# Kernel optimization log

Hardware: AMD Instinct MI355X
Metric: run time of the kernel (lower is better)

## Reference

```python
import jax, jax.numpy as jnp
import numpy as np

N_CLASS, N_SUPPORT, N_QUERY = 64, 5, 64
D_IN, C, WIN = 1024, 128, 5
D = C * WIN * WIN  # 3200, fine-encoder output dim


def setup_inputs() -> dict:
    key = jax.random.key(0)
    ks = jax.random.split(key, 6)
    s = 0.02  # weight init scale
    return {
        "xs": jax.random.normal(ks[0], (N_CLASS, N_SUPPORT, D_IN), jnp.float32),
        "xq": jax.random.normal(ks[1], (N_CLASS, N_QUERY, D_IN), jnp.float32),
        "W_share": jax.random.normal(ks[2], (D_IN, D), jnp.float32) * s,
        "b_share": jnp.zeros((D,), jnp.float32),
        "W_att": jax.random.normal(ks[3], (C, C), jnp.float32) * s,
        "b_att": jnp.zeros((C,), jnp.float32),
        "W_fine": jax.random.normal(ks[4], (D, D), jnp.float32) * s,
        "b_fine": jnp.zeros((D,), jnp.float32),
    }


def reference(xs, xq, W_share, b_share, W_att, b_att, W_fine, b_fine):
    n_class, n_support = xs.shape[0], xs.shape[1]
    n_query = xq.shape[1]
    ns = n_class * n_support

    # concat support + query, run shared encoder
    x = jnp.concatenate([xs.reshape(ns, -1), xq.reshape(n_class * n_query, -1)], axis=0)
    z_share = jax.nn.relu(x @ W_share + b_share)            # [N, D]
    z4 = z_share.reshape(-1, C, WIN, WIN)

    # attention head: spatial mean -> linear -> per-channel logits
    z_att = z4.mean(axis=(2, 3)) @ W_att + b_att            # [N, C]

    diag_c = jax.nn.softmax(z_att[:ns].mean(axis=0)) * C    # [C]
    w = jnp.repeat(diag_c, WIN * WIN)                       # [D] diagonal of learned metric

    # fine encoder (flatten + linear)
    z = z_share @ W_fine + b_fine                           # [N, D]
    z_proto = z[:ns].reshape(n_class, n_support, -1).mean(axis=1)  # [n_class, D]
    zq = z[ns:]                                             # [n, D]

    # attentionMetric with diagonal metric == weighted squared distance:
    # dists[i,j] = sum_d w_d (zq_i - proto_j)^2, expanded to avoid the n*m*d diff tensor
    q2 = (zq * zq) @ w                                      # [n]
    p2 = (z_proto * z_proto) @ w                            # [m]
    cross = (zq * w) @ z_proto.T                            # [n, m]
    dists = q2[:, None] + p2[None, :] - 2.0 * cross         # [n, m]

    log_p_y = jax.nn.log_softmax(-dists, axis=1).reshape(n_class, n_query, n_class)
    target = jnp.arange(n_class)
    tgt = jnp.broadcast_to(target[:, None, None], (n_class, n_query, 1))
    loss_val = -jnp.take_along_axis(log_p_y, tgt, axis=2).mean()
    y_hat = jnp.argmax(log_p_y, axis=2)
    acc_val = (y_hat == target[:, None]).astype(jnp.float32).mean()
    return loss_val, acc_val
```

## Files before the change

### kernel.cpp

```cpp
#include <hip/hip_runtime.h>
#include <math.h>

#define N_CLASS 64
#define N_SUPPORT 5
#define N_QUERY 64
#define D_IN 1024
#define C_CH 128
#define WIN 5
#define D_FEAT 3200
#define NS 320
#define NQ 4096
#define M_ROWS 4416
#define M_PAD 4480

#define ZP_SLICE  (N_CLASS * D_FEAT)
#define GT_SLICE  (128 * D_FEAT)
#define CR_SLICE  (NQ * 128)
#define NKS       10
#define LOSS_BLKS (NQ / 4)

#define PREP_X   4480
#define PREP_WS  800
#define CONV64   2500
#define GEMM8_BLKS (35 * 25)

#define WS_SCALE    64.0f
#define WS_INVSCALE 0.015625f

#define WS_XF8      0u
#define WS_WSF8     4718592u
#define WS_ZSB      8126464u
#define WS_WFB      36388864u
#define WS_WFTB     56868864u
#define WS_ARENA    77348864u
#define WS_UB       98320384u
#define WS_YB       99139584u
#define WS_GT       99958784u
#define WS_WV       100777984u
#define WS_P2       100790784u
#define WS_CVEC     100791296u
#define WS_LPART    100791808u
#define WS_UPOOL    100800128u


typedef __bf16 bf16x8 __attribute__((ext_vector_type(8)));
typedef __bf16 bf16x4 __attribute__((ext_vector_type(4)));
typedef float floatx4 __attribute__((ext_vector_type(4)));
typedef __attribute__((address_space(1))) const void* gptr_t;
typedef __attribute__((address_space(3))) void* lptr_t;

__device__ __forceinline__ float waveReduceSum(float v) {
    for (int off = 32; off > 0; off >>= 1) v += __shfl_xor(v, off, 64);
    return v;
}

__global__ __launch_bounds__(256) void prep_kernel(const float* __restrict__ xs,
                                                   const float* __restrict__ xq,
                                                   const float* __restrict__ W_share,
                                                   unsigned char* __restrict__ Xf8,
                                                   unsigned char* __restrict__ Wsf8)
{
    __shared__ float tile[64][65];
    const int b = blockIdx.x;
    const int t = threadIdx.x;

    if (b < PREP_X) {
        const int e = (b * 256 + t) * 4;
        const int row = e >> 10;
        const int col = e & 1023;
        float4 v = make_float4(0.f, 0.f, 0.f, 0.f);
        if (row < NS)          v = *(const float4*)(xs + (size_t)row * D_IN + col);
        else if (row < M_ROWS) v = *(const float4*)(xq + (size_t)(row - NS) * D_IN + col);
        int p = __builtin_amdgcn_cvt_pk_fp8_f32(v.x, v.y, 0, false);
        p     = __builtin_amdgcn_cvt_pk_fp8_f32(v.z, v.w, p, true);
        const int ocol = col ^ (((row >> 1) & 1) << 3);
        *(int*)(Xf8 + (size_t)row * D_IN + ocol) = p;
        return;
    }
    const int tx = t & 63;
    const int ty = t >> 6;
    const int tb = b - PREP_X;
    const int n0 = (tb % 50) * 64;
    const int k0 = (tb / 50) * 64;
#pragma unroll
    for (int i = ty; i < 64; i += 4)
        tile[i][tx] = W_share[(size_t)(k0 + i) * D_FEAT + n0 + tx];
    __syncthreads();
#pragma unroll
    for (int i = ty; i < 64; i += 4) {
        const int p = __builtin_amdgcn_cvt_pk_fp8_f32(tile[tx][i] * WS_SCALE, 0.f,
                                                      0, false);
        const int n = n0 + i;
        const int k = (k0 + tx) ^ (((n >> 1) & 1) << 3);
        Wsf8[(size_t)n * D_IN + k] = (unsigned char)(p & 0xff);
    }
}

__global__ __launch_bounds__(256, 3) void gemm_fp8_128(const unsigned char* __restrict__ A,
                                                       const unsigned char* __restrict__ Bt,
                                                       const float* __restrict__ bias,
                                                       __bf16* __restrict__ out_bf)
{
    __shared__ __align__(16) unsigned char smem[49152];

    const int t    = threadIdx.x;
    const int lane = t & 63;
    const int w    = t >> 6;
    const int wm   = w >> 1;
    const int wn   = w & 1;

    const int bx = blockIdx.x % 25;
    const int by = blockIdx.x / 25;
    const int bm = by * 128;
    const int bn = bx * 128;

    const int q    = lane >> 4;
    const int r16  = lane & 15;
    const int m3   = (r16 >> 1) & 7;
    const int off0 = (q ^ m3) * 8;

    const int rowA = (wm * 64 + r16) * 64;
    const int rowB = (wn * 64 + r16) * 64;

    const int srow  = t >> 2;
    const int sunit = 16 * ((t & 3) ^ ((srow >> 2) & 3));

    const unsigned char* gA = A  + (size_t)(bm + srow) * D_IN + sunit;
    const unsigned char* gB = Bt + (size_t)(bn + srow) * D_IN + sunit;

    auto stage = [&](int uu, int slot) {
        const unsigned char* ga = gA + uu * 64;
        const unsigned char* gb = gB + uu * 64;
        unsigned char* l = smem + slot * 16384 + t * 16;
        __builtin_amdgcn_global_load_lds((gptr_t)ga,           (lptr_t)l,            16, 0, 0);
        __builtin_amdgcn_global_load_lds((gptr_t)(ga + 65536), (lptr_t)(l + 4096),   16, 0, 0);
        __builtin_amdgcn_global_load_lds((gptr_t)gb,           (lptr_t)(l + 8192),   16, 0, 0);
        __builtin_amdgcn_global_load_lds((gptr_t)(gb + 65536), (lptr_t)(l + 12288),  16, 0, 0);
    };

    floatx4 acc[4][4] = {};
    long av0[4], bv0[4], av1[4], bv1[4];

    auto ld16 = [&](const unsigned char* sa) {
#pragma unroll
        for (int mi = 0; mi < 4; ++mi)
            av0[mi] = *(const long*)(sa + rowA + mi * 1024 + off0);
#pragma unroll
        for (int ni = 0; ni < 4; ++ni)
            bv0[ni] = *(const long*)(sa + 8192 + rowB + ni * 1024 + off0);
#pragma unroll
        for (int mi = 0; mi < 4; ++mi)
            av1[mi] = *(const long*)(sa + rowA + mi * 1024 + (off0 ^ 32));
#pragma unroll
        for (int ni = 0; ni < 4; ++ni)
            bv1[ni] = *(const long*)(sa + 8192 + rowB + ni * 1024 + (off0 ^ 32));
    };
    auto mfma32 = [&]() {
        __builtin_amdgcn_s_setprio(1);
#pragma unroll
        for (int mi = 0; mi < 4; ++mi)
#pragma unroll
            for (int ni = 0; ni < 4; ++ni)
                acc[mi][ni] = __builtin_amdgcn_mfma_f32_16x16x32_fp8_fp8(
                    av0[mi], bv0[ni], acc[mi][ni], 0, 0, 0);
#pragma unroll
        for (int mi = 0; mi < 4; ++mi)
#pragma unroll
            for (int ni = 0; ni < 4; ++ni)
                acc[mi][ni] = __builtin_amdgcn_mfma_f32_16x16x32_fp8_fp8(
                    av1[mi], bv1[ni], acc[mi][ni], 0, 0, 0);
        __builtin_amdgcn_s_setprio(0);
    };

    stage(0, 0);
    stage(1, 1);

    for (int u = 0; u < 14; ++u) {
        const unsigned char* sa = smem + (u % 3) * 16384;
        asm volatile("s_waitcnt vmcnt(4)" ::: "memory");
        __builtin_amdgcn_s_barrier();
        ld16(sa);
        stage(u + 2, (u + 2) % 3);
        asm volatile("s_waitcnt lgkmcnt(0)" ::: "memory");
        mfma32();
    }
    {
        const unsigned char* sa = smem + (14 % 3) * 16384;
        asm volatile("s_waitcnt vmcnt(4)" ::: "memory");
        __builtin_amdgcn_s_barrier();
        ld16(sa);
        asm volatile("s_waitcnt lgkmcnt(0)" ::: "memory");
        mfma32();
    }
    {
        const unsigned char* sa = smem + (15 % 3) * 16384;
        asm volatile("s_waitcnt vmcnt(0)" ::: "memory");
        __builtin_amdgcn_s_barrier();
        ld16(sa);
        asm volatile("s_waitcnt lgkmcnt(0)" ::: "memory");
        mfma32();
    }

    __syncthreads();
    float bcol[4];
#pragma unroll
    for (int ni = 0; ni < 4; ++ni) bcol[ni] = bias[bn + wn * 64 + ni * 16 + r16];
    const int ebase = (wm * 64 + q * 4) * 256 + wn * 128 + r16 * 2;
#pragma unroll
    for (int mi = 0; mi < 4; ++mi)
#pragma unroll
        for (int ni = 0; ni < 4; ++ni) {
            const int cb2 = (ni ^ q) << 5;
#pragma unroll
            for (int reg = 0; reg < 4; ++reg) {
                float v = acc[mi][ni][reg] * WS_INVSCALE + bcol[ni];
                v = fmaxf(v, 0.f);
                *(__bf16*)(smem + ebase + mi * 4096 + reg * 256 + cb2) = (__bf16)v;
            }
        }
    __syncthreads();
#pragma unroll
    for (int ps = 0; ps < 8; ++ps) {
        const int idx  = ps * 256 + t;
        const int row  = idx >> 4;
        const int grow = bm + row;
        if (grow < M_ROWS) {
            const int lb = row * 256 + (((idx & 15) << 4) ^ (((row >> 2) & 3) << 5));
            const int4 d = *(const int4*)(smem + lb);
            *(int4*)((char*)out_bf + ((size_t)grow * D_FEAT + bn + (idx & 15) * 8) * 2) = d;
        }
    }
}

__global__ __launch_bounds__(256) void gemm_bf16(const __bf16* __restrict__ A,
                                                 const __bf16* __restrict__ Bt,
                                                 const float* __restrict__ bias,
                                                 __bf16* __restrict__ out_bf,
                                                 float* __restrict__ out_f32,
                                                 int N, int strideK, int kIters,
                                                 int Mout, int relu, int sliceStride,
                                                 int nbx, int nby, int colLimit,
                                                 const float* __restrict__ attUpool,
                                                 const float* __restrict__ W_att,
                                                 const float* __restrict__ b_att,
                                                 float* __restrict__ wvec)
{
    __shared__ __align__(16) char smem[65536];
    const int t = threadIdx.x;

    if (attUpool != nullptr && blockIdx.x == gridDim.x - 1) {
        float* sW   = (float*)smem;
        float* s_pm = (float*)(smem + 16384);
        float* s_at = (float*)(smem + 16384 + 512);
        float* s_dg = (float*)(smem + 16384 + 1024);
        if (t < C_CH) {
            float a = 0.f;
            for (int p = 0; p < N_CLASS; ++p) a += attUpool[(size_t)p * C_CH + t];
            s_pm[t] = a * (1.0f / (N_CLASS * 25));
        }
        __syncthreads();
        float acc = (t < C_CH) ? b_att[t] : 0.f;
#pragma unroll
        for (int qtr = 0; qtr < 4; ++qtr) {
            const float4* src = (const float4*)(W_att + qtr * 32 * C_CH);
            float4* dst = (float4*)sW;
#pragma unroll
            for (int i = 0; i < 4; ++i) dst[i * 256 + t] = src[i * 256 + t];
            __syncthreads();
            if (t < C_CH) {
#pragma unroll
                for (int k = 0; k < 32; ++k)
                    acc += s_pm[qtr * 32 + k] * sW[k * C_CH + t];
            }
            __syncthreads();
        }
        if (t < C_CH) s_at[t] = acc;
        __syncthreads();
        if (t < C_CH) {
            float m = -INFINITY;
            for (int k = 0; k < C_CH; ++k) m = fmaxf(m, s_at[k]);
            float s = 0.f;
            for (int k = 0; k < C_CH; ++k) s += expf(s_at[k] - m);
            s_dg[t] = expf(acc - m) / s * (float)C_CH;
        }
        __syncthreads();
        for (int j = t; j < D_FEAT; j += 256) wvec[j] = s_dg[j / 25];
        return;
    }

    int bx, by, ks;
    {
        const int nbxy = nbx * nby;
        ks = blockIdx.x / nbxy;
        const int b = blockIdx.x - ks * nbxy;
        const int fg = nbx >> 3;
        const int full = fg * 8 * nby;
        if (b < full) {
            const int g = b / (8 * nby);
            const int r = b - g * 8 * nby;
            bx = g * 8 + (r & 7);
            by = r >> 3;
        } else {
            const int rem = nbx - fg * 8;
            const int r = b - full;
            bx = fg * 8 + r % rem;
            by = r / rem;
        }
    }

    const int lane = t & 63;
    const int w    = t >> 6;
    const int wm   = w >> 1;
    const int wn   = w & 1;
    const int bm   = by * 128;
    const int bn   = bx * 128;

    const int q    = lane >> 4;
    const int r16  = lane & 15;
    const int sw   = (r16 >> 1) & 3;
    const int cA   = (q ^ sw) * 8;

    const int srow   = w * 16 + (lane >> 2);
    const int sglob8 = (((lane & 3) ^ ((lane >> 3) & 3))) * 8;

    const int kBase = ks * kIters * 64;
    floatx4 acc[4][4] = {};

    auto stageb = [&](int ki, char* base) {
        const int k0 = kBase + ki * 64;
#pragma unroll
        for (int s = 0; s < 2; ++s) {
#pragma unroll
            for (int j = 0; j < 2; ++j) {
                const __bf16* ga = A  + (size_t)(bm + j * 64 + srow) * strideK
                                      + k0 + s * 32 + sglob8;
                const __bf16* gb = Bt + (size_t)(bn + j * 64 + srow) * strideK
                                      + k0 + s * 32 + sglob8;
                char* la = base +         s * 8192 + (j * 256 + w * 64) * 16;
                char* lb = base + 16384 + s * 8192 + (j * 256 + w * 64) * 16;
                __builtin_amdgcn_global_load_lds((gptr_t)ga, (lptr_t)la, 16, 0, 0);
                __builtin_amdgcn_global_load_lds((gptr_t)gb, (lptr_t)lb, 16, 0, 0);
            }
        }
    };

    stageb(0, smem);
    for (int ki = 0; ki < kIters; ++ki) {
        char* base = smem + (ki & 1) * 32768;
        __syncthreads();
        if (ki + 1 < kIters) stageb(ki + 1, smem + ((ki + 1) & 1) * 32768);

#pragma unroll
        for (int s = 0; s < 2; ++s) {
            const __bf16* sAe = (const __bf16*)(base +         s * 8192);
            const __bf16* sBe = (const __bf16*)(base + 16384 + s * 8192);
            bf16x8 av[4], bv[4];
#pragma unroll
            for (int mi = 0; mi < 4; ++mi)
                av[mi] = *(const bf16x8*)(sAe + ((wm * 64 + mi * 16 + r16) * 32 + cA));
#pragma unroll
            for (int ni = 0; ni < 4; ++ni)
                bv[ni] = *(const bf16x8*)(sBe + ((wn * 64 + ni * 16 + r16) * 32 + cA));
#pragma unroll
            for (int mi = 0; mi < 4; ++mi)
#pragma unroll
                for (int ni = 0; ni < 4; ++ni)
                    acc[mi][ni] = __builtin_amdgcn_mfma_f32_16x16x32_bf16(
                        av[mi], bv[ni], acc[mi][ni], 0, 0, 0);
        }
    }

#pragma unroll
    for (int ni = 0; ni < 4; ++ni) {
        const int col = bn + wn * 64 + ni * 16 + r16;
        if (col < colLimit) {
            const float bcol = sliceStride ? 0.f : bias[col];
#pragma unroll
            for (int mi = 0; mi < 4; ++mi) {
#pragma unroll
                for (int reg = 0; reg < 4; ++reg) {
                    const int row = bm + wm * 64 + mi * 16 + q * 4 + reg;
                    if (row < Mout) {
                        if (sliceStride) {
                            out_f32[(size_t)ks * sliceStride + (size_t)row * N + col] =
                                acc[mi][ni][reg];
                        } else {
                            float v = acc[mi][ni][reg] + bcol;
                            if (relu) v = fmaxf(v, 0.f);
                            if (out_f32) out_f32[(size_t)row * N + col] = v;
                            else         out_bf [(size_t)row * N + col] = (__bf16)v;
                        }
                    }
                }
            }
        }
    }
}

__global__ __launch_bounds__(256) void ut_conv_kernel(const __bf16* __restrict__ z_share,
                                                      const float* __restrict__ W_fine,
                                                      __bf16* __restrict__ u,
                                                      float* __restrict__ upool,
                                                      __bf16* __restrict__ Wfb,
                                                      __bf16* __restrict__ WfTb)
{
    __shared__ __align__(16) char smem_u[16640];
    const int b = blockIdx.x;
    const int t = threadIdx.x;

    if (b >= 128) {
        float (*tile)[65] = (float(*)[65])smem_u;
        const int tb = b - 128;
        const int tx = t & 63;
        const int ty = t >> 6;
        const int n0 = (tb % 50) * 64;
        const int k0 = (tb / 50) * 64;
#pragma unroll
        for (int i = ty; i < 64; i += 4) {
            const float v = W_fine[(size_t)(k0 + i) * D_FEAT + n0 + tx];
            Wfb[(size_t)(k0 + i) * D_FEAT + n0 + tx] = (__bf16)v;
            tile[i][tx] = v;
        }
        __syncthreads();
#pragma unroll
        for (int i = ty; i < 64; i += 4)
            WfTb[(size_t)(n0 + i) * D_FEAT + k0 + tx] = (__bf16)tile[tx][i];
        return;
    }

    float* srow_ = (float*)smem_u;
    const int p = b;
    if (p >= N_CLASS) {
        for (int k = t; k < D_FEAT; k += 256) u[(size_t)p * D_FEAT + k] = (__bf16)0.f;
        return;
    }
    const __bf16* base = z_share + (size_t)(p * N_SUPPORT) * D_FEAT;
    for (int k = t; k < D_FEAT; k += 256) {
        float s = 0.f;
#pragma unroll
        for (int ss = 0; ss < N_SUPPORT; ++ss) s += (float)base[(size_t)ss * D_FEAT + k];
        s *= (1.0f / N_SUPPORT);
        u[(size_t)p * D_FEAT + k] = (__bf16)s;
        srow_[k] = s;
    }
    __syncthreads();
    if (t < C_CH) {
        float pool = 0.f;
#pragma unroll
        for (int win = 0; win < 25; ++win) pool += srow_[t * 25 + win];
        upool[(size_t)p * C_CH + t] = pool;
    }
}

__global__ __launch_bounds__(256) void y_kernel(const float* __restrict__ zp_part,
                                                const float* __restrict__ wv,
                                                const float* __restrict__ bf,
                                                __bf16* __restrict__ y,
                                                float* __restrict__ p2,
                                                float* __restrict__ cvec)
{
    __shared__ float s_red2[8];
    const int p = blockIdx.x;
    const int t = threadIdx.x;
    if (p >= N_CLASS) {
        for (int j = t; j < D_FEAT; j += 256) y[(size_t)p * D_FEAT + j] = (__bf16)0.f;
        return;
    }
    float s2 = 0.f, sc = 0.f;
    for (int j = t; j < D_FEAT; j += 256) {
        float zpf = bf[j];
#pragma unroll
        for (int ss = 0; ss < NKS; ++ss)
            zpf += zp_part[(size_t)ss * ZP_SLICE + (size_t)p * D_FEAT + j];
        const float wj = wv[j];
        y[(size_t)p * D_FEAT + j] = (__bf16)(wj * zpf);
        s2 += wj * zpf * zpf;
        sc += bf[j] * wj * zpf;
    }
    s2 = waveReduceSum(s2);
    sc = waveReduceSum(sc);
    const int lane = t & 63, wid = t >> 6;
    if (lane == 0) { s_red2[wid] = s2; s_red2[4 + wid] = sc; }
    __syncthreads();
    if (t == 0) {
        p2[p]   = s_red2[0] + s_red2[1] + s_red2[2] + s_red2[3];
        cvec[p] = s_red2[4] + s_red2[5] + s_red2[6] + s_red2[7];
    }
}

__global__ __launch_bounds__(256) void gtsum_kernel(const float* __restrict__ gp,
                                                    __bf16* __restrict__ Gt)
{
    const int i4 = blockIdx.x * 256 + threadIdx.x;
    if (i4 >= GT_SLICE / 4) return;
    float4 s = make_float4(0.f, 0.f, 0.f, 0.f);
#pragma unroll
    for (int ss = 0; ss < NKS; ++ss) {
        const float4 v = *(const float4*)(gp + (size_t)ss * GT_SLICE + i4 * 4);
        s.x += v.x; s.y += v.y; s.z += v.z; s.w += v.w;
    }
    bf16x4 o = { (__bf16)s.x, (__bf16)s.y, (__bf16)s.z, (__bf16)s.w };
    *(bf16x4*)(Gt + (size_t)i4 * 4) = o;
}

__global__ __launch_bounds__(256) void loss_kernel(const float* __restrict__ cross_part,
                                                   const float* __restrict__ p2,
                                                   const float* __restrict__ cvec,
                                                   float* __restrict__ lpart)
{
    __shared__ float s_l[4], s_a[4];
    const int t = threadIdx.x;
    const int lane = t & 63, wid = t >> 6;
    const int i = blockIdx.x * 4 + wid;
    float cr = 0.f;
#pragma unroll
    for (int ss = 0; ss < NKS; ++ss)
        cr += cross_part[(size_t)ss * CR_SLICE + (size_t)i * 128 + lane];
    const float neg = 2.0f * (cr + cvec[lane]) - p2[lane];
    float m = neg;
    for (int off = 32; off > 0; off >>= 1) m = fmaxf(m, __shfl_xor(m, off, 64));
    float e = expf(neg - m);
    float ssum = e;
    for (int off = 32; off > 0; off >>= 1) ssum += __shfl_xor(ssum, off, 64);
    const float lse = m + logf(ssum);
    const int tcls = i >> 6;
    const float negt = __shfl(neg, tcls, 64);
    float v = -neg; int bi = lane;
    for (int off = 32; off > 0; off >>= 1) {
        const float ov = __shfl_xor(v, off, 64);
        const int   oi = __shfl_xor(bi, off, 64);
        if (ov < v || (ov == v && oi < bi)) { v = ov; bi = oi; }
    }
    if (lane == 0) { s_l[wid] = lse - negt; s_a[wid] = (bi == tcls) ? 1.0f : 0.0f; }
    __syncthreads();
    if (t == 0) {
        lpart[blockIdx.x]             = s_l[0] + s_l[1] + s_l[2] + s_l[3];
        lpart[LOSS_BLKS + blockIdx.x] = s_a[0] + s_a[1] + s_a[2] + s_a[3];
    }
}

__global__ __launch_bounds__(256) void writeout_kernel(const float* __restrict__ lpart,
                                                       float* __restrict__ out)
{
    __shared__ float s_red2[8];
    const int t = threadIdx.x;
    float l = 0.f, a = 0.f;
    for (int k = t; k < LOSS_BLKS; k += 256) {
        l += lpart[k];
        a += lpart[LOSS_BLKS + k];
    }
    l = waveReduceSum(l);
    a = waveReduceSum(a);
    const int lane = t & 63, wid = t >> 6;
    if (lane == 0) { s_red2[wid] = l; s_red2[4 + wid] = a; }
    __syncthreads();
    if (t == 0) {
        out[0] = (s_red2[0] + s_red2[1] + s_red2[2] + s_red2[3]) * (1.0f / NQ);
        out[1] = (s_red2[4] + s_red2[5] + s_red2[6] + s_red2[7]) * (1.0f / NQ);
    }
}

extern "C" void kernel_launch(void* const* d_in, const int* in_sizes, int n_in,
                              void* d_out, int out_size, void* d_ws, size_t ws_size,
                              hipStream_t stream)
{
    const float* xs      = (const float*)d_in[0];
    const float* xq      = (const float*)d_in[1];
    const float* W_share = (const float*)d_in[2];
    const float* b_share = (const float*)d_in[3];
    const float* W_att   = (const float*)d_in[4];
    const float* b_att   = (const float*)d_in[5];
    const float* W_fine  = (const float*)d_in[6];
    const float* b_fine  = (const float*)d_in[7];
    float* out = (float*)d_out;

    char* ws = (char*)d_ws;
    unsigned char* Xf8  = (unsigned char*)(ws + WS_XF8);
    unsigned char* Wsf8 = (unsigned char*)(ws + WS_WSF8);
    __bf16* Zsb     = (__bf16*)(ws + WS_ZSB);
    __bf16* Wfb     = (__bf16*)(ws + WS_WFB);
    __bf16* WfTb    = (__bf16*)(ws + WS_WFTB);
    float*  arena   = (float*) (ws + WS_ARENA);
    float*  zp_part = arena;
    float*  gt_part = arena;
    float*  cr_part = arena;
    __bf16* ub      = (__bf16*)(ws + WS_UB);
    __bf16* yb      = (__bf16*)(ws + WS_YB);
    __bf16* Gt      = (__bf16*)(ws + WS_GT);
    float*  wv      = (float*) (ws + WS_WV);
    float*  p2v     = (float*) (ws + WS_P2);
    float*  cvec    = (float*) (ws + WS_CVEC);
    float*  lpart   = (float*) (ws + WS_LPART);
    float*  upool   = (float*) (ws + WS_UPOOL);

    prep_kernel<<<PREP_X + PREP_WS, 256, 0, stream>>>(xs, xq, W_share, Xf8, Wsf8);

    gemm_fp8_128<<<GEMM8_BLKS, 256, 0, stream>>>(Xf8, Wsf8, b_share, Zsb);

    ut_conv_kernel<<<128 + CONV64, 256, 0, stream>>>(Zsb, W_fine, ub, upool,
                                                     Wfb, WfTb);

    gemm_bf16<<<25 * NKS + 1, 256, 0, stream>>>(
        ub, WfTb, nullptr, nullptr, zp_part,
        D_FEAT, D_FEAT, 5, N_CLASS, 0, ZP_SLICE, 25, 1, D_FEAT,
        upool, W_att, b_att, wv);

    y_kernel<<<128, 256, 0, stream>>>(zp_part, wv, b_fine, yb, p2v, cvec);

    gemm_bf16<<<25 * NKS, 256, 0, stream>>>(
        yb, Wfb, nullptr, nullptr, gt_part,
        D_FEAT, D_FEAT, 5, 128, 0, GT_SLICE, 25, 1, D_FEAT,
        nullptr, nullptr, nullptr, nullptr);

    gtsum_kernel<<<(GT_SLICE / 4 + 255) / 256, 256, 0, stream>>>(gt_part, Gt);

    gemm_bf16<<<32 * NKS, 256, 0, stream>>>(
        Zsb + (size_t)NS * D_FEAT, Gt, nullptr, nullptr, cr_part,
        128, D_FEAT, 5, NQ, 0, CR_SLICE, 1, 32, 64,
        nullptr, nullptr, nullptr, nullptr);

    loss_kernel<<<LOSS_BLKS, 256, 0, stream>>>(cr_part, p2v, cvec, lpart);

    writeout_kernel<<<1, 256, 0, stream>>>(lpart, out);
}
```

Baseline: 220.0 us.

## Switch bf16 GEMM to triple-buffered 32-wide K stages with explicit waitcnt

Restructures the bf16 GEMM main loop from double-buffered 64-wide K steps into a three-slot ring of 32-wide K steps, prefetching two stages ahead. Explicit vmcnt/lgkmcnt waits and a raw barrier replace __syncthreads, so loads for stage u+2 are issued while stage u is computed. Shared memory drops from 64KB to 48KB, which may allow more resident blocks. The trade-off is twice as many barriers per K range and reliance on hand-written waitcnt counts being correct.

```diff
diff --git a/kernel.cpp b/kernel.cpp
--- a/kernel.cpp
+++ b/kernel.cpp
@@ -245,7 +245,7 @@
                                                  const float* __restrict__ b_att,
                                                  float* __restrict__ wvec)
 {
-    __shared__ __align__(16) char smem[65536];
+    __shared__ __align__(16) char smem[49152];
     const int t = threadIdx.x;
 
     if (attUpool != nullptr && blockIdx.x == gridDim.x - 1) {
@@ -323,51 +323,59 @@
     const int srow   = w * 16 + (lane >> 2);
     const int sglob8 = (((lane & 3) ^ ((lane >> 3) & 3))) * 8;
 
-    const int kBase = ks * kIters * 64;
+    const int kBase = ks * kIters * 32;
     floatx4 acc[4][4] = {};
 
-    auto stageb = [&](int ki, char* base) {
-        const int k0 = kBase + ki * 64;
-#pragma unroll
-        for (int s = 0; s < 2; ++s) {
-#pragma unroll
-            for (int j = 0; j < 2; ++j) {
-                const __bf16* ga = A  + (size_t)(bm + j * 64 + srow) * strideK
-                                      + k0 + s * 32 + sglob8;
-                const __bf16* gb = Bt + (size_t)(bn + j * 64 + srow) * strideK
-                                      + k0 + s * 32 + sglob8;
-                char* la = base +         s * 8192 + (j * 256 + w * 64) * 16;
-                char* lb = base + 16384 + s * 8192 + (j * 256 + w * 64) * 16;
-                __builtin_amdgcn_global_load_lds((gptr_t)ga, (lptr_t)la, 16, 0, 0);
-                __builtin_amdgcn_global_load_lds((gptr_t)gb, (lptr_t)lb, 16, 0, 0);
-            }
+    auto stageb = [&](int ki, int slot) {
+        const int k0 = kBase + ki * 32;
+        char* base = smem + slot * 16384;
+#pragma unroll
+        for (int j = 0; j < 2; ++j) {
+            const __bf16* ga = A  + (size_t)(bm + j * 64 + srow) * strideK
+                                  + k0 + sglob8;
+            const __bf16* gb = Bt + (size_t)(bn + j * 64 + srow) * strideK
+                                  + k0 + sglob8;
+            char* la = base +        j * 4096 + w * 1024;
+            char* lb = base + 8192 + j * 4096 + w * 1024;
+            __builtin_amdgcn_global_load_lds((gptr_t)ga, (lptr_t)la, 16, 0, 0);
+            __builtin_amdgcn_global_load_lds((gptr_t)gb, (lptr_t)lb, 16, 0, 0);
         }
     };
 
-    stageb(0, smem);
-    for (int ki = 0; ki < kIters; ++ki) {
-        char* base = smem + (ki & 1) * 32768;
-        __syncthreads();
-        if (ki + 1 < kIters) stageb(ki + 1, smem + ((ki + 1) & 1) * 32768);
-
-#pragma unroll
-        for (int s = 0; s < 2; ++s) {
-            const __bf16* sAe = (const __bf16*)(base +         s * 8192);
-            const __bf16* sBe = (const __bf16*)(base + 16384 + s * 8192);
-            bf16x8 av[4], bv[4];
-#pragma unroll
-            for (int mi = 0; mi < 4; ++mi)
-                av[mi] = *(const bf16x8*)(sAe + ((wm * 64 + mi * 16 + r16) * 32 + cA));
+    bf16x8 av[4], bv[4];
+    auto ldfrags = [&](const char* base) {
+        const __bf16* sAe = (const __bf16*)base;
+        const __bf16* sBe = (const __bf16*)(base + 8192);
+#pragma unroll
+        for (int mi = 0; mi < 4; ++mi)
+            av[mi] = *(const bf16x8*)(sAe + ((wm * 64 + mi * 16 + r16) * 32 + cA));
+#pragma unroll
+        for (int ni = 0; ni < 4; ++ni)
+            bv[ni] = *(const bf16x8*)(sBe + ((wn * 64 + ni * 16 + r16) * 32 + cA));
+    };
+    auto mfma16 = [&]() {
+#pragma unroll
+        for (int mi = 0; mi < 4; ++mi)
 #pragma unroll
             for (int ni = 0; ni < 4; ++ni)
-                bv[ni] = *(const bf16x8*)(sBe + ((wn * 64 + ni * 16 + r16) * 32 + cA));
-#pragma unroll
-            for (int mi = 0; mi < 4; ++mi)
-#pragma unroll
-                for (int ni = 0; ni < 4; ++ni)
-                    acc[mi][ni] = __builtin_amdgcn_mfma_f32_16x16x32_bf16(
-                        av[mi], bv[ni], acc[mi][ni], 0, 0, 0);
-        }
+                acc[mi][ni] = __builtin_amdgcn_mfma_f32_16x16x32_bf16(
+                    av[mi], bv[ni], acc[mi][ni], 0, 0, 0);
+    };
+
+    stageb(0, 0);
+    stageb(1, 1);
+
+    for (int u = 0; u < kIters; ++u) {
+        const char* base = smem + (u % 3) * 16384;
+        if (u + 1 < kIters)
+            asm volatile("s_waitcnt vmcnt(4)" ::: "memory");
+        else
+            asm volatile("s_waitcnt vmcnt(0)" ::: "memory");
+        __builtin_amdgcn_s_barrier();
+        ldfrags(base);
+        if (u + 2 < kIters) stageb(u + 2, (u + 2) % 3);
+        asm volatile("s_waitcnt lgkmcnt(0)" ::: "memory");
+        mfma16();
     }
 
 #pragma unroll
@@ -602,21 +610,21 @@
 
     gemm_bf16<<<25 * NKS + 1, 256, 0, stream>>>(
         ub, WfTb, nullptr, nullptr, zp_part,
-        D_FEAT, D_FEAT, 5, N_CLASS, 0, ZP_SLICE, 25, 1, D_FEAT,
+        D_FEAT, D_FEAT, 10, N_CLASS, 0, ZP_SLICE, 25, 1, D_FEAT,
         upool, W_att, b_att, wv);
 
     y_kernel<<<128, 256, 0, stream>>>(zp_part, wv, b_fine, yb, p2v, cvec);
 
     gemm_bf16<<<25 * NKS, 256, 0, stream>>>(
         yb, Wfb, nullptr, nullptr, gt_part,
-        D_FEAT, D_FEAT, 5, 128, 0, GT_SLICE, 25, 1, D_FEAT,
+        D_FEAT, D_FEAT, 10, 128, 0, GT_SLICE, 25, 1, D_FEAT,
         nullptr, nullptr, nullptr, nullptr);
 
     gtsum_kernel<<<(GT_SLICE / 4 + 255) / 256, 256, 0, stream>>>(gt_part, Gt);
 
     gemm_bf16<<<32 * NKS, 256, 0, stream>>>(
         Zsb + (size_t)NS * D_FEAT, Gt, nullptr, nullptr, cr_part,
-        128, D_FEAT, 5, NQ, 0, CR_SLICE, 1, 32, 64,
+        128, D_FEAT, 10, NQ, 0, CR_SLICE, 1, 32, 64,
         nullptr, nullptr, nullptr, nullptr);
 
     loss_kernel<<<LOSS_BLKS, 256, 0, stream>>>(cr_part, p2v, cvec, lpart);
```

Result: no change. 217.5 us (-1.2%).
